# Optimization experiments

Measured on AMD Instinct MI355X. Metric: run time of the kernel, lower is better.

The kernel has to match this reference:

```python
import jax, jax.numpy as jnp
import numpy as np

CHANNELS = 64
HIDDEN = 1024
LAYERS = 24
NODE_TYPES = 19
BN_EPS = 1e-5

N_NODES = 200000
N_EDGES = 800000
N_RULES = 50000


def setup_inputs() -> dict:
    key = jax.random.key(0)
    ks = jax.random.split(key, 16)
    nodes = jax.random.randint(ks[0], (N_NODES,), 0, NODE_TYPES)
    sources = jax.random.randint(ks[1], (N_EDGES,), 0, N_NODES)
    targets = jax.random.randint(ks[2], (N_EDGES,), 0, N_NODES)
    rules = jax.random.randint(ks[3], (N_RULES,), 0, N_NODES)
    f32 = jnp.float32
    emb = jax.random.normal(ks[4], (NODE_TYPES, CHANNELS), f32)
    # per-layer, per-direction (out/back) Conv params, stacked [LAYERS, 2, ...]
    W = jax.random.normal(ks[5], (LAYERS, 2, CHANNELS, CHANNELS), f32) * 0.125  # ~xavier
    b = jax.random.normal(ks[6], (LAYERS, 2, CHANNELS), f32) * 0.01
    gamma = 1.0 + 0.1 * jax.random.normal(ks[7], (LAYERS, 2, CHANNELS), f32)
    beta = 0.01 * jax.random.normal(ks[8], (LAYERS, 2, CHANNELS), f32)
    rmean = 0.01 * jax.random.normal(ks[9], (LAYERS, 2, CHANNELS), f32)
    rvar = jax.random.uniform(ks[10], (LAYERS, 2, CHANNELS), f32, 0.5, 1.5)
    Wh = jax.random.normal(ks[11], (HIDDEN, CHANNELS), f32) * 0.05
    bh = jax.random.normal(ks[12], (HIDDEN,), f32) * 0.01
    Wo = jax.random.normal(ks[13], (1, HIDDEN), f32) * 0.03
    return {"nodes": nodes, "sources": sources, "targets": targets, "rules": rules,
            "emb": emb, "W": W, "b": b, "gamma": gamma, "beta": beta,
            "rmean": rmean, "rvar": rvar, "Wh": Wh, "bh": bh, "Wo": Wo}


def reference(nodes, sources, targets, rules, emb, W, b, gamma, beta, rmean, rvar, Wh, bh, Wo):
    n = nodes.shape[0]

    def conv(x, src, tgt, Wi, bi, g, be, rm, rv):
        # scatter_mean of gathered source features onto target nodes
        s = jax.ops.segment_sum(x[src], tgt, num_segments=n)            # [n, C]
        cnt = jax.ops.segment_sum(jnp.ones(src.shape, x.dtype), tgt, num_segments=n)
        m = s / jnp.maximum(cnt, 1.0)[:, None]
        # eval-mode BatchNorm1d (running stats) fused as affine
        xn = (m - rm) * (g * jax.lax.rsqrt(rv + BN_EPS)) + be
        return jax.nn.relu(xn @ Wi.T + bi)

    def layer(x, p):
        Wl, bl, gl, bel, rml, rvl = p
        out = conv(x, sources, targets, Wl[0], bl[0], gl[0], bel[0], rml[0], rvl[0])
        back = conv(x, targets, sources, Wl[1], bl[1], gl[1], bel[1], rml[1], rvl[1])
        return x + out + back, None

    x = emb[nodes]                                                      # [n, C]
    x, _ = jax.lax.scan(layer, x, (W, b, gamma, beta, rmean, rvar))
    h = jax.nn.relu(x[rules] @ Wh.T + bh)                               # [R, HIDDEN]
    return (h @ Wo.T)[:, 0]                                             # [R]
```

## Files before the change

kernel.cpp:

```cpp
#include <hip/hip_runtime.h>

#define N_NODES 200000
#define N_EDGES 800000
#define N_RULES 50000
#define NLAYERS 24
#define SCAN_NB 196
#define RP_STRIDE 200064

typedef short bf16x8 __attribute__((ext_vector_type(8)));
typedef float floatx4 __attribute__((ext_vector_type(4)));

__device__ __forceinline__ unsigned short f2bf(float f) {
  unsigned int b = __float_as_uint(f);
  b += 0x7FFFu + ((b >> 16) & 1u);
  return (unsigned short)(b >> 16);
}
__device__ __forceinline__ float bf2f(unsigned short u) {
  return __uint_as_float(((unsigned int)u) << 16);
}


__global__ void k_hist(const int* __restrict__ src, const int* __restrict__ tgt,
                       int* __restrict__ deg_out, int* __restrict__ deg_back,
                       int* __restrict__ rank_out, int* __restrict__ rank_back) {
  int e = blockIdx.x * 256 + threadIdx.x;
  rank_out[e]  = atomicAdd(&deg_out[tgt[e]], 1);
  rank_back[e] = atomicAdd(&deg_back[src[e]], 1);
}

__global__ void k_scanA(const int* __restrict__ deg, int* __restrict__ part) {
  int y = blockIdx.y;
  const int* d = deg + y * N_NODES;
  __shared__ int sh[256];
  int t = threadIdx.x;
  int base = blockIdx.x * 1024 + t * 4;
  int s = 0;
  #pragma unroll
  for (int k = 0; k < 4; ++k) { int i = base + k; if (i < N_NODES) s += d[i]; }
  sh[t] = s; __syncthreads();
  for (int off = 128; off > 0; off >>= 1) { if (t < off) sh[t] += sh[t + off]; __syncthreads(); }
  if (t == 0) part[y * SCAN_NB + blockIdx.x] = sh[0];
}

__global__ void k_scanB(int* __restrict__ part, int* __restrict__ rp) {
  int y = blockIdx.y;
  __shared__ int buf[256];
  int t = threadIdx.x;
  int v = (t < SCAN_NB) ? part[y * SCAN_NB + t] : 0;
  buf[t] = v; __syncthreads();
  for (int off = 1; off < 256; off <<= 1) {
    int x = (t >= off) ? buf[t - off] : 0;
    __syncthreads();
    buf[t] += x;
    __syncthreads();
  }
  if (t < SCAN_NB) part[y * SCAN_NB + t] = buf[t] - v;
  if (t == 0) rp[y * RP_STRIDE + N_NODES] = N_EDGES;
}

__global__ void k_scanC(const int* __restrict__ deg, const int* __restrict__ part,
                        int* __restrict__ rp) {
  int y = blockIdx.y;
  const int* d = deg + y * N_NODES;
  int* r = rp + y * RP_STRIDE;
  __shared__ int buf[256];
  int t = threadIdx.x;
  int base = blockIdx.x * 1024 + t * 4;
  int dv[4]; int s = 0;
  #pragma unroll
  for (int k = 0; k < 4; ++k) { int i = base + k; dv[k] = (i < N_NODES) ? d[i] : 0; s += dv[k]; }
  buf[t] = s; __syncthreads();
  int sv = s;
  for (int off = 1; off < 256; off <<= 1) {
    int x = (t >= off) ? buf[t - off] : 0;
    __syncthreads();
    buf[t] += x;
    __syncthreads();
  }
  int e = part[y * SCAN_NB + blockIdx.x] + buf[t] - sv;
  #pragma unroll
  for (int k = 0; k < 4; ++k) { int i = base + k; if (i < N_NODES) r[i] = e; e += dv[k]; }
}

__global__ void k_fill(const int* __restrict__ src, const int* __restrict__ tgt,
                       const int* __restrict__ rp_out, const int* __restrict__ rp_back,
                       const int* __restrict__ rank_out, const int* __restrict__ rank_back,
                       int* __restrict__ ci_out, int* __restrict__ ci_back) {
  int e = blockIdx.x * 256 + threadIdx.x;
  int s = src[e], t = tgt[e];
  ci_out[rp_out[t] + rank_out[e]] = s;
  ci_back[rp_back[s] + rank_back[e]] = t;
}

__global__ void k_prep(const float* __restrict__ W, const float* __restrict__ b,
                       const float* __restrict__ gamma, const float* __restrict__ beta,
                       const float* __restrict__ rmean, const float* __restrict__ rvar,
                       unsigned short* __restrict__ WpF, float* __restrict__ bp) {
  int d = blockIdx.x, l = blockIdx.y, lane = threadIdx.x;
  int ld = l * 2 + d;
  __shared__ float s_s[64], t_s[64];
  float s = gamma[ld * 64 + lane] * rsqrtf(rvar[ld * 64 + lane] + 1e-5f);
  s_s[lane] = s;
  t_s[lane] = beta[ld * 64 + lane] - rmean[ld * 64 + lane] * s;
  __syncthreads();
  float bias = b[ld * 64 + lane];
  for (int j = 0; j < 64; ++j) bias += W[(ld * 64 + lane) * 64 + j] * t_s[j];
  bp[ld * 64 + lane] = bias;
  #pragma unroll
  for (int f = 0; f < 8; ++f) {
    int ct = f >> 1, kh = f & 1;
    int row = ct * 16 + (lane & 15);
    #pragma unroll
    for (int jj = 0; jj < 8; ++jj) {
      int k = kh * 32 + (lane >> 4) * 8 + jj;
      float val = W[(ld * 64 + row) * 64 + k] * s_s[k];
      WpF[(ld * 8 + f) * 512 + lane * 8 + jj] = f2bf(val);
    }
  }
}

__global__ void k_prep2(const float* __restrict__ Wh,
                        unsigned short* __restrict__ WhFhi,
                        unsigned short* __restrict__ WhFlo) {
  int jt = blockIdx.x, lane = threadIdx.x;
  #pragma unroll
  for (int kh = 0; kh < 2; ++kh) {
    #pragma unroll
    for (int jj = 0; jj < 8; ++jj) {
      int j = jt * 16 + (lane & 15);
      int k = kh * 32 + (lane >> 4) * 8 + jj;
      float wv = Wh[j * 64 + k];
      unsigned short hi = f2bf(wv);
      WhFhi[(jt * 2 + kh) * 512 + lane * 8 + jj] = hi;
      WhFlo[(jt * 2 + kh) * 512 + lane * 8 + jj] = f2bf(wv - bf2f(hi));
    }
  }
}

__global__ void k_embed(const int* __restrict__ nodes, const float* __restrict__ emb,
                        unsigned short* __restrict__ hi_a,
                        unsigned short* __restrict__ lo) {
  int gid = blockIdx.x * 256 + threadIdx.x;
  int i = gid >> 6, c = gid & 63;
  float v = emb[nodes[i] * 64 + c];
  unsigned short h = f2bf(v);
  hi_a[gid] = h;
  lo[gid] = f2bf(v - bf2f(h));
}

__global__ __launch_bounds__(256) void k_layer(
    const unsigned short* __restrict__ hi_in,
    unsigned short* __restrict__ hi_out,
    unsigned short* __restrict__ lo,
    const int* __restrict__ rp0, const int* __restrict__ ci0,
    const int* __restrict__ rp1, const int* __restrict__ ci1,
    const unsigned short* __restrict__ WfL, const float* __restrict__ bpL) {
  __shared__ __align__(16) unsigned short m_s[4][16 * 72];
  __shared__ __align__(16) float y_s[4][16 * 68];
  __shared__ float bp_s[128];
  int tid = threadIdx.x, lane = tid & 63, w = tid >> 6;
  if (tid < 128) bp_s[tid] = bpL[tid];
  __syncthreads();
  int base = (blockIdx.x * 4 + w) * 16;
  int n15 = lane & 15, q = lane >> 4;

  int rpv0 = (lane < 17) ? rp0[base + lane] : 0;
  int rpv1 = (lane < 17) ? rp1[base + lane] : 0;
  int rs0 = __builtin_amdgcn_readlane(rpv0, 0);
  int re0 = __builtin_amdgcn_readlane(rpv0, 16);
  int rs1 = __builtin_amdgcn_readlane(rpv1, 0);
  int re1 = __builtin_amdgcn_readlane(rpv1, 16);
  int cv0 = (rs0 + lane < re0) ? ci0[rs0 + lane] : 0;
  int cv1 = (rs1 + lane < re1) ? ci1[rs1 + lane] : 0;

#define ACCUM16(buf, jbase)                                               \
  _Pragma("unroll")                                                       \
  for (int u = 0; u < 16; ++u) {                                          \
    int j = (jbase) + u;                                                  \
    if (j < ce) {                                                         \
      while (j >= cend) {                                                 \
        int deg = cend - cstart;                                          \
        float invc = deg > 0 ? __builtin_amdgcn_rcpf((float)deg) : 0.f;   \
        m_s[w][cur * 72 + lane] = f2bf(acc * invc);                       \
        acc = 0.f; cur++; cstart = cend;                                  \
        cend = __builtin_amdgcn_readlane(rpv, cur + 1);                   \
      }                                                                   \
      acc += buf[u];                                                      \
    }                                                                     \
  }

  for (int d = 0; d < 2; ++d) {
    const int* ci = d ? ci1 : ci0;
    int rpv = d ? rpv1 : rpv0;
    int rs  = d ? rs1  : rs0;
    int re  = d ? re1  : re0;
    int cv  = d ? cv1  : cv0;
    int cur = 0;
    int cstart = rs;
    int cend = __builtin_amdgcn_readlane(rpv, 1);
    float acc = 0.f;

    for (int cb = rs; cb < re; cb += 64) {
      int ce = (cb + 64 < re) ? cb + 64 : re;
      int cv_next = (cb + 64 + lane < re) ? ci[cb + 64 + lane] : 0;
      float v[16], vn[16];
      #pragma unroll
      for (int u = 0; u < 16; ++u) {
        int sn = __builtin_amdgcn_readlane(cv, u);
        v[u] = bf2f(hi_in[sn * 64 + lane]);
      }
      for (int j0 = cb; j0 < ce; j0 += 32) {
        if (j0 + 16 < ce) {
          #pragma unroll
          for (int u = 0; u < 16; ++u) {
            int sn = __builtin_amdgcn_readlane(cv, j0 - cb + 16 + u);
            vn[u] = bf2f(hi_in[sn * 64 + lane]);
          }
        }
        ACCUM16(v, j0)
        if (j0 + 32 < ce) {
          #pragma unroll
          for (int u = 0; u < 16; ++u) {
            int sn = __builtin_amdgcn_readlane(cv, j0 - cb + 32 + u);
            v[u] = bf2f(hi_in[sn * 64 + lane]);
          }
        }
        if (j0 + 16 < ce) {
          ACCUM16(vn, j0 + 16)
        }
      }
      cv = cv_next;
    }
    #pragma unroll 1
    while (cur < 16) {
      int deg = cend - cstart;
      float invc = deg > 0 ? __builtin_amdgcn_rcpf((float)deg) : 0.f;
      m_s[w][cur * 72 + lane] = f2bf(acc * invc);
      acc = 0.f; cstart = cend; cur++;
      if (cur < 16) cend = __builtin_amdgcn_readlane(rpv, cur + 1);
    }

    const unsigned short* wf = WfL + d * 4096;
    bf16x8 b0 = *(const bf16x8*)&m_s[w][n15 * 72 + q * 8];
    bf16x8 b1 = *(const bf16x8*)&m_s[w][n15 * 72 + 32 + q * 8];
    #pragma unroll
    for (int ct = 0; ct < 4; ++ct) {
      floatx4 d4 = {0.f, 0.f, 0.f, 0.f};
      bf16x8 a0 = *(const bf16x8*)(wf + (ct * 2 + 0) * 512 + lane * 8);
      bf16x8 a1 = *(const bf16x8*)(wf + (ct * 2 + 1) * 512 + lane * 8);
      d4 = __builtin_amdgcn_mfma_f32_16x16x32_bf16(a0, b0, d4, 0, 0, 0);
      d4 = __builtin_amdgcn_mfma_f32_16x16x32_bf16(a1, b1, d4, 0, 0, 0);
      floatx4 yv;
      #pragma unroll
      for (int i = 0; i < 4; ++i)
        yv[i] = fmaxf(d4[i] + bp_s[d * 64 + ct * 16 + q * 4 + i], 0.f);
      float* yp = &y_s[w][n15 * 68 + ct * 16 + q * 4];
      if (d == 0) {
        *(floatx4*)yp = yv;
      } else {
        floatx4 o = *(const floatx4*)yp;
        o += yv;
        *(floatx4*)yp = o;
      }
    }
  }
#undef ACCUM16

  #pragma unroll
  for (int r = 0; r < 16; ++r) {
    int gi = (base + r) * 64 + lane;
    float xv = bf2f(hi_in[gi]) + bf2f(lo[gi]) + y_s[w][r * 68 + lane];
    unsigned short h = f2bf(xv);
    hi_out[gi] = h;
    lo[gi] = f2bf(xv - bf2f(h));
  }
}

__global__ __launch_bounds__(256) void k_final(
    const unsigned short* __restrict__ hi, const unsigned short* __restrict__ lo,
    const int* __restrict__ rules,
    const unsigned short* __restrict__ WhFhi, const unsigned short* __restrict__ WhFlo,
    const float* __restrict__ bh, const float* __restrict__ Wo,
    float* __restrict__ out) {
  __shared__ __align__(16) float bh_s[1024], wo_s[1024];
  int tid = threadIdx.x, lane = tid & 63, w = tid >> 6;
  ((floatx4*)bh_s)[tid] = ((const floatx4*)bh)[tid];
  ((floatx4*)wo_s)[tid] = ((const floatx4*)Wo)[tid];
  __syncthreads();
  int n15 = lane & 15, q = lane >> 4;
  int rbase = (blockIdx.x * 4 + w) * 16;
  int ru = rbase + n15;
  int nd = rules[ru < N_RULES ? ru : N_RULES - 1];
  bf16x8 b0h = *(const bf16x8*)&hi[nd * 64 + q * 8];
  bf16x8 b1h = *(const bf16x8*)&hi[nd * 64 + 32 + q * 8];
  bf16x8 b0l = *(const bf16x8*)&lo[nd * 64 + q * 8];
  bf16x8 b1l = *(const bf16x8*)&lo[nd * 64 + 32 + q * 8];
  float acc = 0.f;
  #pragma unroll 4
  for (int jt = 0; jt < 64; ++jt) {
    const unsigned short* fh = WhFhi + (jt * 2) * 512 + lane * 8;
    const unsigned short* fl = WhFlo + (jt * 2) * 512 + lane * 8;
    bf16x8 a0h = *(const bf16x8*)fh;
    bf16x8 a1h = *(const bf16x8*)(fh + 512);
    bf16x8 a0l = *(const bf16x8*)fl;
    bf16x8 a1l = *(const bf16x8*)(fl + 512);
    floatx4 d4 = {0.f, 0.f, 0.f, 0.f};
    d4 = __builtin_amdgcn_mfma_f32_16x16x32_bf16(a0h, b0h, d4, 0, 0, 0);
    d4 = __builtin_amdgcn_mfma_f32_16x16x32_bf16(a1h, b1h, d4, 0, 0, 0);
    d4 = __builtin_amdgcn_mfma_f32_16x16x32_bf16(a0h, b0l, d4, 0, 0, 0);
    d4 = __builtin_amdgcn_mfma_f32_16x16x32_bf16(a1h, b1l, d4, 0, 0, 0);
    d4 = __builtin_amdgcn_mfma_f32_16x16x32_bf16(a0l, b0h, d4, 0, 0, 0);
    d4 = __builtin_amdgcn_mfma_f32_16x16x32_bf16(a1l, b1h, d4, 0, 0, 0);
    floatx4 bh4 = *(const floatx4*)&bh_s[jt * 16 + q * 4];
    floatx4 wo4 = *(const floatx4*)&wo_s[jt * 16 + q * 4];
    #pragma unroll
    for (int i = 0; i < 4; ++i)
      acc += fmaxf(d4[i] + bh4[i], 0.f) * wo4[i];
  }
  acc += __shfl_down(acc, 32);
  acc += __shfl_down(acc, 16);
  if (lane < 16 && rbase + lane < N_RULES) out[rbase + lane] = acc;
}

extern "C" void kernel_launch(void* const* d_in, const int* in_sizes, int n_in,
                              void* d_out, int out_size, void* d_ws, size_t ws_size,
                              hipStream_t stream) {
  const int* nodes = (const int*)d_in[0];
  const int* sources = (const int*)d_in[1];
  const int* targets = (const int*)d_in[2];
  const int* rules = (const int*)d_in[3];
  const float* emb = (const float*)d_in[4];
  const float* W = (const float*)d_in[5];
  const float* b = (const float*)d_in[6];
  const float* gamma = (const float*)d_in[7];
  const float* beta = (const float*)d_in[8];
  const float* rmean = (const float*)d_in[9];
  const float* rvar = (const float*)d_in[10];
  const float* Wh = (const float*)d_in[11];
  const float* bh = (const float*)d_in[12];
  const float* Wo = (const float*)d_in[13];
  float* out = (float*)d_out;

  if (ws_size < 95100000u) return;

  char* ws = (char*)d_ws;
  unsigned short* hi_a = (unsigned short*)(ws + 0);
  unsigned short* hi_b = (unsigned short*)(ws + 25600000);
  unsigned short* lo   = (unsigned short*)(ws + 51200000);
  int* deg_out  = (int*)(ws + 76800000);
  int* deg_back = (int*)(ws + 77600000);
  int* rank_out = (int*)(ws + 78400000);
  int* rank_back= (int*)(ws + 81600000);
  int* rp_out   = (int*)(ws + 84800000);
  int* rp_back  = (int*)(ws + 85600256);
  int* ci_out   = (int*)(ws + 86400512);
  int* ci_back  = (int*)(ws + 89600512);
  int* part     = (int*)(ws + 92800512);
  unsigned short* WpF   = (unsigned short*)(ws + 92802080);
  float* bp             = (float*)(ws + 93195296);
  unsigned short* WhFhi = (unsigned short*)(ws + 93207584);
  unsigned short* WhFlo = (unsigned short*)(ws + 93338656);

  (void)hipMemsetAsync(deg_out, 0, 1600000u, stream);

  k_hist<<<3125, 256, 0, stream>>>(sources, targets, deg_out, deg_back,
                                   rank_out, rank_back);
  k_scanA<<<dim3(SCAN_NB, 2), 256, 0, stream>>>(deg_out, part);
  k_scanB<<<dim3(1, 2), 256, 0, stream>>>(part, rp_out);
  k_scanC<<<dim3(SCAN_NB, 2), 256, 0, stream>>>(deg_out, part, rp_out);
  k_fill<<<3125, 256, 0, stream>>>(sources, targets, rp_out, rp_back,
                                   rank_out, rank_back, ci_out, ci_back);
  k_prep<<<dim3(2, NLAYERS), 64, 0, stream>>>(W, b, gamma, beta, rmean, rvar, WpF, bp);
  k_prep2<<<64, 64, 0, stream>>>(Wh, WhFhi, WhFlo);
  k_embed<<<50000, 256, 0, stream>>>(nodes, emb, hi_a, lo);

  const unsigned short* hin = hi_a;
  unsigned short* hout = hi_b;
  for (int l = 0; l < NLAYERS; ++l) {
    k_layer<<<3125, 256, 0, stream>>>(hin, hout, lo,
                                      rp_out, ci_out, rp_back, ci_back,
                                      WpF + (size_t)l * 8192, bp + (size_t)l * 128);
    const unsigned short* tmp = hin; hin = hout; hout = (unsigned short*)tmp;
  }
  k_final<<<782, 256, 0, stream>>>(hin, lo, rules, WhFhi, WhFlo, bh, Wo, out);
}
```

Measured before the change: 1.813 ms.

## Drop y_s staging, apply residual from MFMA registers, simplify gather pipeline

Removes the float y_s shared buffer. Both directions' mean aggregates are now kept in separate m_s slices, and both MFMA products are computed after aggregation. The residual update is applied straight from MFMA accumulator registers with vectorized 4-wide bf16 loads and stores, instead of going through shared memory in a row loop. The double-buffered 16-neighbor prefetch is replaced by a single 16-wide gather batch, and launch bounds request 8 blocks per CU. The goal is lower LDS and register use to raise occupancy, trading away explicit software prefetch of gathers.

```diff
diff --git a/kernel.cpp b/kernel.cpp
--- a/kernel.cpp
+++ b/kernel.cpp
@@ -9,6 +9,7 @@
 
 typedef short bf16x8 __attribute__((ext_vector_type(8)));
 typedef float floatx4 __attribute__((ext_vector_type(4)));
+typedef unsigned short ushort4v __attribute__((ext_vector_type(4)));
 
 __device__ __forceinline__ unsigned short f2bf(float f) {
   unsigned int b = __float_as_uint(f);
@@ -148,15 +149,14 @@
   lo[gid] = f2bf(v - bf2f(h));
 }
 
-__global__ __launch_bounds__(256) void k_layer(
+__global__ __launch_bounds__(256, 8) void k_layer(
     const unsigned short* __restrict__ hi_in,
     unsigned short* __restrict__ hi_out,
     unsigned short* __restrict__ lo,
     const int* __restrict__ rp0, const int* __restrict__ ci0,
     const int* __restrict__ rp1, const int* __restrict__ ci1,
     const unsigned short* __restrict__ WfL, const float* __restrict__ bpL) {
-  __shared__ __align__(16) unsigned short m_s[4][16 * 72];
-  __shared__ __align__(16) float y_s[4][16 * 68];
+  __shared__ __align__(16) unsigned short m_s[2][4][16 * 72];
   __shared__ float bp_s[128];
   int tid = threadIdx.x, lane = tid & 63, w = tid >> 6;
   if (tid < 128) bp_s[tid] = bpL[tid];
@@ -173,28 +173,13 @@
   int cv0 = (rs0 + lane < re0) ? ci0[rs0 + lane] : 0;
   int cv1 = (rs1 + lane < re1) ? ci1[rs1 + lane] : 0;
 
-#define ACCUM16(buf, jbase)                                               \
-  _Pragma("unroll")                                                       \
-  for (int u = 0; u < 16; ++u) {                                          \
-    int j = (jbase) + u;                                                  \
-    if (j < ce) {                                                         \
-      while (j >= cend) {                                                 \
-        int deg = cend - cstart;                                          \
-        float invc = deg > 0 ? __builtin_amdgcn_rcpf((float)deg) : 0.f;   \
-        m_s[w][cur * 72 + lane] = f2bf(acc * invc);                       \
-        acc = 0.f; cur++; cstart = cend;                                  \
-        cend = __builtin_amdgcn_readlane(rpv, cur + 1);                   \
-      }                                                                   \
-      acc += buf[u];                                                      \
-    }                                                                     \
-  }
-
   for (int d = 0; d < 2; ++d) {
     const int* ci = d ? ci1 : ci0;
     int rpv = d ? rpv1 : rpv0;
     int rs  = d ? rs1  : rs0;
     int re  = d ? re1  : re0;
     int cv  = d ? cv1  : cv0;
+    unsigned short* md = &m_s[d][w][0];
     int cur = 0;
     int cstart = rs;
     int cend = __builtin_amdgcn_readlane(rpv, 1);
@@ -203,30 +188,26 @@
     for (int cb = rs; cb < re; cb += 64) {
       int ce = (cb + 64 < re) ? cb + 64 : re;
       int cv_next = (cb + 64 + lane < re) ? ci[cb + 64 + lane] : 0;
-      float v[16], vn[16];
-      #pragma unroll
-      for (int u = 0; u < 16; ++u) {
-        int sn = __builtin_amdgcn_readlane(cv, u);
-        v[u] = bf2f(hi_in[sn * 64 + lane]);
-      }
-      for (int j0 = cb; j0 < ce; j0 += 32) {
-        if (j0 + 16 < ce) {
-          #pragma unroll
-          for (int u = 0; u < 16; ++u) {
-            int sn = __builtin_amdgcn_readlane(cv, j0 - cb + 16 + u);
-            vn[u] = bf2f(hi_in[sn * 64 + lane]);
+      for (int j0 = cb; j0 < ce; j0 += 16) {
+        float v[16];
+        #pragma unroll
+        for (int u = 0; u < 16; ++u) {
+          int sn = __builtin_amdgcn_readlane(cv, j0 + u - cb);
+          v[u] = bf2f(hi_in[sn * 64 + lane]);
+        }
+        #pragma unroll
+        for (int u = 0; u < 16; ++u) {
+          int j = j0 + u;
+          if (j < ce) {
+            while (j >= cend) {
+              int deg = cend - cstart;
+              float invc = deg > 0 ? __builtin_amdgcn_rcpf((float)deg) : 0.f;
+              md[cur * 72 + lane] = f2bf(acc * invc);
+              acc = 0.f; cur++; cstart = cend;
+              cend = __builtin_amdgcn_readlane(rpv, cur + 1);
+            }
+            acc += v[u];
           }
-        }
-        ACCUM16(v, j0)
-        if (j0 + 32 < ce) {
-          #pragma unroll
-          for (int u = 0; u < 16; ++u) {
-            int sn = __builtin_amdgcn_readlane(cv, j0 - cb + 32 + u);
-            v[u] = bf2f(hi_in[sn * 64 + lane]);
-          }
-        }
-        if (j0 + 16 < ce) {
-          ACCUM16(vn, j0 + 16)
         }
       }
       cv = cv_next;
@@ -235,44 +216,42 @@
     while (cur < 16) {
       int deg = cend - cstart;
       float invc = deg > 0 ? __builtin_amdgcn_rcpf((float)deg) : 0.f;
-      m_s[w][cur * 72 + lane] = f2bf(acc * invc);
+      md[cur * 72 + lane] = f2bf(acc * invc);
       acc = 0.f; cstart = cend; cur++;
       if (cur < 16) cend = __builtin_amdgcn_readlane(rpv, cur + 1);
     }
-
-    const unsigned short* wf = WfL + d * 4096;
-    bf16x8 b0 = *(const bf16x8*)&m_s[w][n15 * 72 + q * 8];
-    bf16x8 b1 = *(const bf16x8*)&m_s[w][n15 * 72 + 32 + q * 8];
+  }
+
+  bf16x8 b0d0 = *(const bf16x8*)&m_s[0][w][n15 * 72 + q * 8];
+  bf16x8 b1d0 = *(const bf16x8*)&m_s[0][w][n15 * 72 + 32 + q * 8];
+  bf16x8 b0d1 = *(const bf16x8*)&m_s[1][w][n15 * 72 + q * 8];
+  bf16x8 b1d1 = *(const bf16x8*)&m_s[1][w][n15 * 72 + 32 + q * 8];
+  #pragma unroll
+  for (int ct = 0; ct < 4; ++ct) {
+    const unsigned short* wf0 = WfL + (ct * 2) * 512 + lane * 8;
+    const unsigned short* wf1 = WfL + 4096 + (ct * 2) * 512 + lane * 8;
+    floatx4 d40 = {0.f, 0.f, 0.f, 0.f};
+    floatx4 d41 = {0.f, 0.f, 0.f, 0.f};
+    d40 = __builtin_amdgcn_mfma_f32_16x16x32_bf16(*(const bf16x8*)wf0, b0d0, d40, 0, 0, 0);
+    d40 = __builtin_amdgcn_mfma_f32_16x16x32_bf16(*(const bf16x8*)(wf0 + 512), b1d0, d40, 0, 0, 0);
+    d41 = __builtin_amdgcn_mfma_f32_16x16x32_bf16(*(const bf16x8*)wf1, b0d1, d41, 0, 0, 0);
+    d41 = __builtin_amdgcn_mfma_f32_16x16x32_bf16(*(const bf16x8*)(wf1 + 512), b1d1, d41, 0, 0, 0);
+    int c0 = ct * 16 + q * 4;
+    int gi = (base + n15) * 64 + c0;
+    ushort4v hv = *(const ushort4v*)&hi_in[gi];
+    ushort4v lv = *(const ushort4v*)&lo[gi];
+    ushort4v ho, lno;
     #pragma unroll
-    for (int ct = 0; ct < 4; ++ct) {
-      floatx4 d4 = {0.f, 0.f, 0.f, 0.f};
-      bf16x8 a0 = *(const bf16x8*)(wf + (ct * 2 + 0) * 512 + lane * 8);
-      bf16x8 a1 = *(const bf16x8*)(wf + (ct * 2 + 1) * 512 + lane * 8);
-      d4 = __builtin_amdgcn_mfma_f32_16x16x32_bf16(a0, b0, d4, 0, 0, 0);
-      d4 = __builtin_amdgcn_mfma_f32_16x16x32_bf16(a1, b1, d4, 0, 0, 0);
-      floatx4 yv;
-      #pragma unroll
-      for (int i = 0; i < 4; ++i)
-        yv[i] = fmaxf(d4[i] + bp_s[d * 64 + ct * 16 + q * 4 + i], 0.f);
-      float* yp = &y_s[w][n15 * 68 + ct * 16 + q * 4];
-      if (d == 0) {
-        *(floatx4*)yp = yv;
-      } else {
-        floatx4 o = *(const floatx4*)yp;
-        o += yv;
-        *(floatx4*)yp = o;
-      }
-    }
-  }
-#undef ACCUM16
-
-  #pragma unroll
-  for (int r = 0; r < 16; ++r) {
-    int gi = (base + r) * 64 + lane;
-    float xv = bf2f(hi_in[gi]) + bf2f(lo[gi]) + y_s[w][r * 68 + lane];
-    unsigned short h = f2bf(xv);
-    hi_out[gi] = h;
-    lo[gi] = f2bf(xv - bf2f(h));
+    for (int i = 0; i < 4; ++i) {
+      float yv = fmaxf(d40[i] + bp_s[c0 + i], 0.f)
+               + fmaxf(d41[i] + bp_s[64 + c0 + i], 0.f);
+      float xv = bf2f(hv[i]) + bf2f(lv[i]) + yv;
+      unsigned short h = f2bf(xv);
+      ho[i] = h;
+      lno[i] = f2bf(xv - bf2f(h));
+    }
+    *(ushort4v*)&hi_out[gi] = ho;
+    *(ushort4v*)&lo[gi] = lno;
   }
 }
 
```

Result: slower. 1.894 ms (+4.5%).
